# Optimization experiments

Hardware: AMD Instinct MI355X
Metric: run time of the kernel (lower is better)

Reference implementation:

```python
import jax, jax.numpy as jnp
import numpy as np

BN_EPS = 1e-5
Q_EPS = 1e-8

def quant_weight(w):
    # per-output-channel median-abs scale, ternary quantization
    s = jnp.median(jnp.abs(w).reshape(w.shape[0], -1), axis=1)
    s = jnp.maximum(s, Q_EPS)[:, None, None, None]
    return jnp.clip(jnp.round(w / s), -1.0, 1.0) * s

def bitconv(x, w, b, stride, pad):
    wq = quant_weight(w)
    y = jax.lax.conv_general_dilated(
        x, wq, (stride, stride), [(pad, pad), (pad, pad)],
        dimension_numbers=('NCHW', 'OIHW', 'NCHW'))
    return y + b[None, :, None, None]

def bn(x, g, b, m, v):
    scale = g / jnp.sqrt(v + BN_EPS)
    return x * scale[None, :, None, None] + (b - m * scale)[None, :, None, None]

def setup_inputs() -> dict:
    key = jax.random.key(0)
    ks = jax.random.split(key, 20)
    B, Cin, H, W = 64, 1024, 14, 14
    width, Cout = 256, 1024  # planes=256, expansion=4
    d = {}
    d['x'] = jax.random.normal(ks[0], (B, Cin, H, W), jnp.float32)
    d['w1'] = jax.random.normal(ks[1], (width, Cin, 1, 1), jnp.float32) * 0.05
    d['b1'] = jax.random.normal(ks[2], (width,), jnp.float32) * 0.01
    d['g1'] = jax.random.uniform(ks[3], (width,), jnp.float32, 0.5, 1.5)
    d['be1'] = jax.random.normal(ks[4], (width,), jnp.float32) * 0.1
    d['m1'] = jax.random.normal(ks[5], (width,), jnp.float32) * 0.1
    d['v1'] = jax.random.uniform(ks[6], (width,), jnp.float32, 0.5, 1.5)
    d['w2'] = jax.random.normal(ks[7], (width, width, 3, 3), jnp.float32) * 0.05
    d['b2'] = jax.random.normal(ks[8], (width,), jnp.float32) * 0.01
    d['g2'] = jax.random.uniform(ks[9], (width,), jnp.float32, 0.5, 1.5)
    d['be2'] = jax.random.normal(ks[10], (width,), jnp.float32) * 0.1
    d['m2'] = jax.random.normal(ks[11], (width,), jnp.float32) * 0.1
    d['v2'] = jax.random.uniform(ks[12], (width,), jnp.float32, 0.5, 1.5)
    d['w3'] = jax.random.normal(ks[13], (Cout, width, 1, 1), jnp.float32) * 0.05
    d['b3'] = jax.random.normal(ks[14], (Cout,), jnp.float32) * 0.01
    d['g3'] = jax.random.uniform(ks[15], (Cout,), jnp.float32, 0.5, 1.5)
    d['be3'] = jax.random.normal(ks[16], (Cout,), jnp.float32) * 0.1
    d['m3'] = jax.random.normal(ks[17], (Cout,), jnp.float32) * 0.1
    d['v3'] = jax.random.uniform(ks[18], (Cout,), jnp.float32, 0.5, 1.5)
    return d

def reference(x, w1, b1, g1, be1, m1, v1,
              w2, b2, g2, be2, m2, v2,
              w3, b3, g3, be3, m3, v3):
    out = jax.nn.silu(bn(bitconv(x, w1, b1, 1, 0), g1, be1, m1, v1))
    out = jax.nn.silu(bn(bitconv(out, w2, b2, 1, 1), g2, be2, m2, v2))
    out = bn(bitconv(out, w3, b3, 1, 0), g3, be3, m3, v3)
    return jax.nn.silu(out + x)
```

## Files before the change

### kernel.cpp

```cpp
#include <hip/hip_runtime.h>
#include <cstdint>
#include <cstddef>

typedef unsigned short u16;
typedef unsigned int u32;
typedef __attribute__((ext_vector_type(4))) float f32x4;
typedef __attribute__((ext_vector_type(8))) short s16x8;

__device__ __forceinline__ u16 f2bf(float f) {
  u32 u = __float_as_uint(f);
  u = (u + 0x7fffu + ((u >> 16) & 1u)) >> 16;
  return (u16)u;
}

__device__ __forceinline__ float silu_f(float y) {
  return y / (1.0f + __expf(-y));
}

__device__ __forceinline__ void gl_lds16(const u16* g, u16* l) {
  __builtin_amdgcn_global_load_lds(
      (const __attribute__((address_space(1))) void*)g,
      (__attribute__((address_space(3))) void*)l, 16, 0, 0);
}

template<int N, int REMAP>
__global__ __launch_bounds__(64) void quant_kernel(
    const float* __restrict__ w, const float* __restrict__ bias,
    const float* __restrict__ g, const float* __restrict__ be,
    const float* __restrict__ mu, const float* __restrict__ var,
    u16* __restrict__ wq, float* __restrict__ alpha, float* __restrict__ beta)
{
  constexpr int NV = N / 64;
  __shared__ int hist[256];

  const int lane = threadIdx.x;
  const int ch = blockIdx.x;

  u32 vals[NV];
  const float* wp = w + (size_t)ch * N;
  #pragma unroll
  for (int t = 0; t < NV; ++t)
    vals[t] = __float_as_uint(wp[lane + 64 * t]);

  const int r0 = N / 2;
  int r = r0;
  u32 prefix = 0;
  #pragma unroll
  for (int pass = 0; pass < 4; ++pass) {
    const int shift = 24 - 8 * pass;
    hist[lane] = 0;
    hist[64 + lane] = 0;
    hist[128 + lane] = 0;
    hist[192 + lane] = 0;
    __syncthreads();
    #pragma unroll
    for (int t = 0; t < NV; ++t) {
      u32 a = vals[t] & 0x7fffffffu;
      bool cand;
      if (pass == 0) cand = true;
      else cand = ((a >> (shift + 8)) == (prefix >> (shift + 8)));
      if (cand) atomicAdd(&hist[(a >> shift) & 255], 1);
    }
    __syncthreads();
    int h0 = hist[4 * lane + 0];
    int h1 = hist[4 * lane + 1];
    int h2 = hist[4 * lane + 2];
    int h3 = hist[4 * lane + 3];
    int s4 = h0 + h1 + h2 + h3;
    int cum = s4;
    #pragma unroll
    for (int off = 1; off < 64; off <<= 1) {
      int tt = __shfl_up(cum, off);
      if (lane >= off) cum += tt;
    }
    int pre = cum - s4;
    bool sel = (r > pre) && (r <= cum);
    unsigned long long bal = __ballot(sel);
    int src = __ffsll((unsigned long long)bal) - 1;
    int c0 = pre + h0, c1 = c0 + h1, c2 = c1 + h2;
    int d_l, nr_l;
    if (r <= c0)      { d_l = 4 * lane + 0; nr_l = r - pre; }
    else if (r <= c1) { d_l = 4 * lane + 1; nr_l = r - c0; }
    else if (r <= c2) { d_l = 4 * lane + 2; nr_l = r - c1; }
    else              { d_l = 4 * lane + 3; nr_l = r - c2; }
    int d = __shfl(d_l, src);
    r = __shfl(nr_l, src);
    prefix |= (u32)d << shift;
    __syncthreads();
  }
  const u32 v0 = prefix;

  int cle = 0;
  u32 mn = 0xFFFFFFFFu;
  #pragma unroll
  for (int t = 0; t < NV; ++t) {
    u32 a = vals[t] & 0x7fffffffu;
    cle += (a <= v0) ? 1 : 0;
    if (a > v0) mn = min(mn, a);
  }
  #pragma unroll
  for (int off = 1; off < 64; off <<= 1) {
    cle += __shfl_xor(cle, off);
    mn = min(mn, (u32)__shfl_xor((int)mn, off));
  }
  u32 v1 = (cle >= r0 + 1) ? v0 : mn;

  float s = 0.5f * (__uint_as_float(v0) + __uint_as_float(v1));
  s = fmaxf(s, 1e-8f);

  #pragma unroll
  for (int t = 0; t < NV; ++t) {
    int i = lane + 64 * t;
    float q = rintf(__uint_as_float(vals[t]) / s);
    q = fminf(fmaxf(q, -1.0f), 1.0f);
    int oi;
    if (REMAP) {
      int cin = i / 9, tap = i - cin * 9;
      oi = tap * 256 + cin;
    } else {
      oi = i;
    }
    wq[(size_t)ch * N + oi] = f2bf(q);
  }
  if (lane == 0) {
    float sc = g[ch] / sqrtf(var[ch] + 1e-5f);
    alpha[ch] = s * sc;
    beta[ch] = (bias[ch] - mu[ch]) * sc + be[ch];
  }
}

__global__ __launch_bounds__(256) void transpose_cast_kernel(
    const float* __restrict__ x, u16* __restrict__ xb)
{
  __shared__ u16 tile[64 * 198];
  const int n = blockIdx.x;
  const int c0 = blockIdx.y * 64;
  const float* xp = x + ((size_t)n * 1024 + c0) * 196;
  const float4* xp4 = reinterpret_cast<const float4*>(xp);
  for (int i = threadIdx.x; i < 64 * 49; i += 256) {
    int c = i / 49, hg = i - c * 49;
    float4 v = xp4[i];
    u16* t = &tile[c * 198 + hg * 4];
    t[0] = f2bf(v.x); t[1] = f2bf(v.y); t[2] = f2bf(v.z); t[3] = f2bf(v.w);
  }
  __syncthreads();
  u32* op = reinterpret_cast<u32*>(xb + (size_t)n * 196 * 1024 + c0);
  for (int i = threadIdx.x; i < 196 * 32; i += 256) {
    int hw = i >> 5, cp = i & 31;
    u32 lo = tile[(cp * 2) * 198 + hw];
    u32 hi = tile[(cp * 2 + 1) * 198 + hw];
    op[hw * 512 + cp] = lo | (hi << 16);
  }
}

template<int MODE, int KTOT, int BJ>
__global__ __launch_bounds__(256, 2) void gemm_kernel(
    const u16* __restrict__ Wq, const u16* __restrict__ Bact,
    const float* __restrict__ alpha, const float* __restrict__ beta,
    u16* __restrict__ outb, float* __restrict__ outf, const float* __restrict__ xres)
{
  constexpr int BK = 64;
  constexpr int NKT = KTOT / BK;
  constexpr int NI = BJ / 32;
  constexpr int ACH = 4;
  constexpr int BCH = BJ / 32;
  constexpr int SMEM_SIZE = (MODE == 3) ? 34816 : 25600;

  __shared__ __align__(16) char smem[SMEM_SIZE];
  u16* As = (u16*)smem;
  u16* Bs = (u16*)(smem + 16384);
  float* aS = (float*)(MODE == 3 ? (smem + 33792) : (smem + 16384 + BJ * 128));
  float* bS = aS + 128;
  float* lbuf = (float*)smem;

  const int tid = threadIdx.x;
  const int jb = blockIdx.x * BJ;
  const int cb = blockIdx.y * 128;
  const int wave = tid >> 6;
  const int lane = tid & 63;
  const int wm = (wave & 1) * 64;
  const int wn = (wave >> 1) * (BJ / 2);
  const int quad = lane >> 4;
  const int l16 = lane & 15;
  const int lr = lane >> 3;
  const int perm = (lane & 7) ^ lr;

  const u16* gA[ACH];
  #pragma unroll
  for (int it = 0; it < ACH; ++it) {
    int row = wave * 32 + it * 8 + lr;
    gA[it] = Wq + (size_t)(cb + row) * KTOT + perm * 8;
  }
  const u16* gB[BCH];
  #pragma unroll
  for (int it = 0; it < BCH; ++it) {
    int row = wave * (8 * BCH) + it * 8 + lr;
    if (MODE == 2) {
      int j = jb + row;
      int n = j / 196, hw = j - n * 196;
      int h = hw / 14, w = hw - h * 14;
      gB[it] = Bact + (size_t)(((n * 16 + h) * 16 + w) * 256) + perm * 8;
    } else {
      gB[it] = Bact + (size_t)(jb + row) * KTOT + perm * 8;
    }
  }

  if (tid < 128) {
    aS[tid] = alpha[cb + tid];
    bS[tid] = beta[cb + tid];
  }

  f32x4 acc[4][NI];
  #pragma unroll
  for (int a = 0; a < 4; ++a)
    #pragma unroll
    for (int b = 0; b < NI; ++b)
      acc[a][b] = {0.f, 0.f, 0.f, 0.f};

  for (int kt = 0; kt < NKT; ++kt) {
    #pragma unroll
    for (int it = 0; it < ACH; ++it)
      gl_lds16(gA[it] + kt * BK, As + (wave * ACH + it) * 512);
    if (MODE == 2) {
      int tap = kt >> 2;
      int c0 = (kt & 3) * 64;
      int dy = tap / 3, dx = tap - dy * 3;
      int tapoff = (dy * 16 + dx) * 256 + c0;
      #pragma unroll
      for (int it = 0; it < BCH; ++it)
        gl_lds16(gB[it] + tapoff, Bs + (wave * BCH + it) * 512);
    } else {
      #pragma unroll
      for (int it = 0; it < BCH; ++it)
        gl_lds16(gB[it] + kt * BK, Bs + (wave * BCH + it) * 512);
    }
    __syncthreads();

    #pragma unroll
    for (int s = 0; s < 2; ++s) {
      s16x8 af[4], bf[NI];
      #pragma unroll
      for (int mi = 0; mi < 4; ++mi) {
        int row = wm + mi * 16 + l16;
        int kc = s * 4 + quad;
        af[mi] = *reinterpret_cast<const s16x8*>(&As[row * BK + ((kc ^ (row & 7)) << 3)]);
      }
      #pragma unroll
      for (int ni = 0; ni < NI; ++ni) {
        int row = wn + ni * 16 + l16;
        int kc = s * 4 + quad;
        bf[ni] = *reinterpret_cast<const s16x8*>(&Bs[row * BK + ((kc ^ (row & 7)) << 3)]);
      }
      #pragma unroll
      for (int mi = 0; mi < 4; ++mi)
        #pragma unroll
        for (int ni = 0; ni < NI; ++ni)
          acc[mi][ni] = __builtin_amdgcn_mfma_f32_16x16x32_bf16(af[mi], bf[ni], acc[mi][ni], 0, 0, 0);
    }
    __syncthreads();
  }

  if (MODE == 1 || MODE == 2) {
    #pragma unroll
    for (int mi = 0; mi < 4; ++mi) {
      const int lc = wm + mi * 16 + quad * 4;
      #pragma unroll
      for (int ni = 0; ni < NI; ++ni) {
        const int j = jb + wn + ni * 16 + l16;
        ushort4 pk;
        float y;
        y = silu_f(aS[lc + 0] * acc[mi][ni][0] + bS[lc + 0]); pk.x = f2bf(y);
        y = silu_f(aS[lc + 1] * acc[mi][ni][1] + bS[lc + 1]); pk.y = f2bf(y);
        y = silu_f(aS[lc + 2] * acc[mi][ni][2] + bS[lc + 2]); pk.z = f2bf(y);
        y = silu_f(aS[lc + 3] * acc[mi][ni][3] + bS[lc + 3]); pk.w = f2bf(y);
        size_t base;
        if (MODE == 1) {
          int n = j / 196, hw = j - n * 196;
          int h = hw / 14, w = hw - h * 14;
          base = (size_t)(((n * 16 + h + 1) * 16) + (w + 1)) * 256 + cb + lc;
        } else {
          base = (size_t)j * 256 + cb + lc;
        }
        *reinterpret_cast<ushort4*>(&outb[base]) = pk;
      }
    }
  } else {
    #pragma unroll
    for (int k = 0; k < 2; ++k) {
      if ((wave & 1) == k) {
        #pragma unroll
        for (int mi = 0; mi < 4; ++mi) {
          const int cl = mi * 16 + quad * 4;
          const int gc = 64 * k + cl;
          #pragma unroll
          for (int ni = 0; ni < 4; ++ni) {
            const int jj = wn + ni * 16 + l16;
            #pragma unroll
            for (int r = 0; r < 4; ++r)
              lbuf[(cl + r) * 132 + jj] = aS[gc + r] * acc[mi][ni][r] + bS[gc + r];
          }
        }
      }
      __syncthreads();
      #pragma unroll
      for (int it = 0; it < 8; ++it) {
        int idx = tid + it * 256;
        int cl = idx >> 5;
        int jg = idx & 31;
        int c = cb + 64 * k + cl;
        int j0 = jb + jg * 4;
        int n = j0 / 196, hw = j0 - n * 196;
        size_t o = (size_t)n * 200704 + (size_t)c * 196 + hw;
        float4 lv = *reinterpret_cast<float4*>(&lbuf[cl * 132 + jg * 4]);
        float4 xv = *reinterpret_cast<const float4*>(&xres[o]);
        float4 ov;
        ov.x = silu_f(lv.x + xv.x);
        ov.y = silu_f(lv.y + xv.y);
        ov.z = silu_f(lv.z + xv.z);
        ov.w = silu_f(lv.w + xv.w);
        *reinterpret_cast<float4*>(&outf[o]) = ov;
      }
      __syncthreads();
    }
  }
}

extern "C" void kernel_launch(void* const* d_in, const int* in_sizes, int n_in,
                              void* d_out, int out_size, void* d_ws, size_t ws_size,
                              hipStream_t stream)
{
  const float* x   = (const float*)d_in[0];
  const float* w1  = (const float*)d_in[1];
  const float* b1  = (const float*)d_in[2];
  const float* g1  = (const float*)d_in[3];
  const float* be1 = (const float*)d_in[4];
  const float* m1  = (const float*)d_in[5];
  const float* v1  = (const float*)d_in[6];
  const float* w2  = (const float*)d_in[7];
  const float* b2  = (const float*)d_in[8];
  const float* g2  = (const float*)d_in[9];
  const float* be2 = (const float*)d_in[10];
  const float* m2  = (const float*)d_in[11];
  const float* v2  = (const float*)d_in[12];
  const float* w3  = (const float*)d_in[13];
  const float* b3  = (const float*)d_in[14];
  const float* g3  = (const float*)d_in[15];
  const float* be3 = (const float*)d_in[16];
  const float* m3  = (const float*)d_in[17];
  const float* v3  = (const float*)d_in[18];
  float* out = (float*)d_out;

  uint8_t* ws = (uint8_t*)d_ws;
  u16* xb    = (u16*)(ws);
  u16* act1p = (u16*)(ws + 25690112ull);
  u16* act2  = (u16*)(ws + 34078720ull);
  u16* w1q   = (u16*)(ws + 40501248ull);
  u16* w2q   = (u16*)(ws + 41025536ull);
  u16* w3q   = (u16*)(ws + 42205184ull);
  float* a1c = (float*)(ws + 42729472ull);
  float* b1c = a1c + 256;
  float* a2c = b1c + 256;
  float* b2c = a2c + 256;
  float* a3c = b2c + 256;
  float* b3c = a3c + 1024;

  hipMemsetAsync(act1p, 0, 8388608ull, stream);

  transpose_cast_kernel<<<dim3(64, 16), 256, 0, stream>>>(x, xb);
  quant_kernel<1024, 0><<<256, 64, 0, stream>>>(w1, b1, g1, be1, m1, v1, w1q, a1c, b1c);
  quant_kernel<2304, 1><<<256, 64, 0, stream>>>(w2, b2, g2, be2, m2, v2, w2q, a2c, b2c);
  quant_kernel<256, 0><<<1024, 64, 0, stream>>>(w3, b3, g3, be3, m3, v3, w3q, a3c, b3c);

  gemm_kernel<1, 1024, 64><<<dim3(196, 2), 256, 0, stream>>>(w1q, xb, a1c, b1c, act1p, (float*)nullptr, (const float*)nullptr);
  gemm_kernel<2, 2304, 64><<<dim3(196, 2), 256, 0, stream>>>(w2q, act1p, a2c, b2c, act2, (float*)nullptr, (const float*)nullptr);
  gemm_kernel<3, 256, 128><<<dim3(98, 8), 256, 0, stream>>>(w3q, act2, a3c, b3c, (u16*)nullptr, out, x);
}
```

Baseline: 239.5 us.

## Fuse prep kernels into one launch, zero only halo, shrink GEMM tiles

```diff
diff --git a/kernel.cpp b/kernel.cpp
--- a/kernel.cpp
+++ b/kernel.cpp
@@ -24,17 +24,16 @@
 }
 
 template<int N, int REMAP>
-__global__ __launch_bounds__(64) void quant_kernel(
+__device__ void quant_dev(
+    int grp, int wave, int lane, int* hist ,
     const float* __restrict__ w, const float* __restrict__ bias,
     const float* __restrict__ g, const float* __restrict__ be,
     const float* __restrict__ mu, const float* __restrict__ var,
     u16* __restrict__ wq, float* __restrict__ alpha, float* __restrict__ beta)
 {
   constexpr int NV = N / 64;
-  __shared__ int hist[256];
-
-  const int lane = threadIdx.x;
-  const int ch = blockIdx.x;
+  const int ch = grp * 4 + wave;
+  const int wb = wave * 256;
 
   u32 vals[NV];
   const float* wp = w + (size_t)ch * N;
@@ -48,10 +47,10 @@
   #pragma unroll
   for (int pass = 0; pass < 4; ++pass) {
     const int shift = 24 - 8 * pass;
-    hist[lane] = 0;
-    hist[64 + lane] = 0;
-    hist[128 + lane] = 0;
-    hist[192 + lane] = 0;
+    hist[wb + lane] = 0;
+    hist[wb + 64 + lane] = 0;
+    hist[wb + 128 + lane] = 0;
+    hist[wb + 192 + lane] = 0;
     __syncthreads();
     #pragma unroll
     for (int t = 0; t < NV; ++t) {
@@ -59,13 +58,13 @@
       bool cand;
       if (pass == 0) cand = true;
       else cand = ((a >> (shift + 8)) == (prefix >> (shift + 8)));
-      if (cand) atomicAdd(&hist[(a >> shift) & 255], 1);
-    }
-    __syncthreads();
-    int h0 = hist[4 * lane + 0];
-    int h1 = hist[4 * lane + 1];
-    int h2 = hist[4 * lane + 2];
-    int h3 = hist[4 * lane + 3];
+      if (cand) atomicAdd(&hist[wb + ((a >> shift) & 255)], 1);
+    }
+    __syncthreads();
+    int h0 = hist[wb + 4 * lane + 0];
+    int h1 = hist[wb + 4 * lane + 1];
+    int h2 = hist[wb + 4 * lane + 2];
+    int h3 = hist[wb + 4 * lane + 3];
     int s4 = h0 + h1 + h2 + h3;
     int cum = s4;
     #pragma unroll
@@ -129,32 +128,74 @@
   }
 }
 
-__global__ __launch_bounds__(256) void transpose_cast_kernel(
-    const float* __restrict__ x, u16* __restrict__ xb)
+__global__ __launch_bounds__(256) void prep_kernel(
+    const float* __restrict__ x, u16* __restrict__ xb,
+    const float* __restrict__ w1, const float* __restrict__ b1,
+    const float* __restrict__ g1, const float* __restrict__ be1,
+    const float* __restrict__ m1, const float* __restrict__ v1,
+    u16* __restrict__ w1q, float* __restrict__ a1c, float* __restrict__ b1c,
+    const float* __restrict__ w2, const float* __restrict__ b2,
+    const float* __restrict__ g2, const float* __restrict__ be2,
+    const float* __restrict__ m2, const float* __restrict__ v2,
+    u16* __restrict__ w2q, float* __restrict__ a2c, float* __restrict__ b2c,
+    const float* __restrict__ w3, const float* __restrict__ b3,
+    const float* __restrict__ g3, const float* __restrict__ be3,
+    const float* __restrict__ m3, const float* __restrict__ v3,
+    u16* __restrict__ w3q, float* __restrict__ a3c, float* __restrict__ b3c,
+    u16* __restrict__ act1p)
 {
-  __shared__ u16 tile[64 * 198];
-  const int n = blockIdx.x;
-  const int c0 = blockIdx.y * 64;
-  const float* xp = x + ((size_t)n * 1024 + c0) * 196;
-  const float4* xp4 = reinterpret_cast<const float4*>(xp);
-  for (int i = threadIdx.x; i < 64 * 49; i += 256) {
-    int c = i / 49, hg = i - c * 49;
-    float4 v = xp4[i];
-    u16* t = &tile[c * 198 + hg * 4];
-    t[0] = f2bf(v.x); t[1] = f2bf(v.y); t[2] = f2bf(v.z); t[3] = f2bf(v.w);
-  }
-  __syncthreads();
-  u32* op = reinterpret_cast<u32*>(xb + (size_t)n * 196 * 1024 + c0);
-  for (int i = threadIdx.x; i < 196 * 32; i += 256) {
-    int hw = i >> 5, cp = i & 31;
-    u32 lo = tile[(cp * 2) * 198 + hw];
-    u32 hi = tile[(cp * 2 + 1) * 198 + hw];
-    op[hw * 512 + cp] = lo | (hi << 16);
+  __shared__ __align__(16) char smem[25344];
+  const int b = blockIdx.x;
+  const int tid = threadIdx.x;
+  const int wave = tid >> 6;
+  const int lane = tid & 63;
+
+  if (b < 1024) {
+    u16* tile = (u16*)smem;
+    const int n = b >> 4;
+    const int c0 = (b & 15) * 64;
+    const float* xp = x + ((size_t)n * 1024 + c0) * 196;
+    const float4* xp4 = reinterpret_cast<const float4*>(xp);
+    for (int i = tid; i < 64 * 49; i += 256) {
+      int c = i / 49, hg = i - c * 49;
+      float4 v = xp4[i];
+      u16* t = &tile[c * 198 + hg * 4];
+      t[0] = f2bf(v.x); t[1] = f2bf(v.y); t[2] = f2bf(v.z); t[3] = f2bf(v.w);
+    }
+    __syncthreads();
+    u32* op = reinterpret_cast<u32*>(xb + (size_t)n * 196 * 1024 + c0);
+    for (int i = tid; i < 196 * 32; i += 256) {
+      int hw = i >> 5, cp = i & 31;
+      u32 lo = tile[(cp * 2) * 198 + hw];
+      u32 hi = tile[(cp * 2 + 1) * 198 + hw];
+      op[hw * 512 + cp] = lo | (hi << 16);
+    }
+  } else if (b < 1088) {
+    quant_dev<1024, 0>(b - 1024, wave, lane, (int*)smem,
+                       w1, b1, g1, be1, m1, v1, w1q, a1c, b1c);
+  } else if (b < 1152) {
+    quant_dev<2304, 1>(b - 1088, wave, lane, (int*)smem,
+                       w2, b2, g2, be2, m2, v2, w2q, a2c, b2c);
+  } else if (b < 1408) {
+    quant_dev<256, 0>(b - 1152, wave, lane, (int*)smem,
+                      w3, b3, g3, be3, m3, v3, w3q, a3c, b3c);
+  } else {
+    const int n = b - 1408;
+    u32* base = reinterpret_cast<u32*>(act1p + (size_t)n * 16 * 16 * 256);
+    for (int i = tid; i < 7680; i += 256) {
+      int p = i >> 7;
+      int cc = i & 127;
+      int h, w;
+      if (p < 16)      { h = 0;  w = p; }
+      else if (p < 32) { h = 15; w = p - 16; }
+      else { int q = p - 32; h = 1 + (q >> 1); w = (q & 1) * 15; }
+      base[((h * 16 + w) << 7) + cc] = 0u;
+    }
   }
 }
 
 template<int MODE, int KTOT, int BJ>
-__global__ __launch_bounds__(256, 2) void gemm_kernel(
+__global__ __launch_bounds__(256, 4) void gemm_kernel(
     const u16* __restrict__ Wq, const u16* __restrict__ Bact,
     const float* __restrict__ alpha, const float* __restrict__ beta,
     u16* __restrict__ outb, float* __restrict__ outf, const float* __restrict__ xres)
@@ -164,7 +205,7 @@
   constexpr int NI = BJ / 32;
   constexpr int ACH = 4;
   constexpr int BCH = BJ / 32;
-  constexpr int SMEM_SIZE = (MODE == 3) ? 34816 : 25600;
+  constexpr int SMEM_SIZE = (MODE == 3) ? 34816 : (16384 + BJ * 128 + 1024);
 
   __shared__ __align__(16) char smem[SMEM_SIZE];
   u16* As = (u16*)smem;
@@ -364,14 +405,14 @@
   float* a3c = b2c + 256;
   float* b3c = a3c + 1024;
 
-  hipMemsetAsync(act1p, 0, 8388608ull, stream);
-
-  transpose_cast_kernel<<<dim3(64, 16), 256, 0, stream>>>(x, xb);
-  quant_kernel<1024, 0><<<256, 64, 0, stream>>>(w1, b1, g1, be1, m1, v1, w1q, a1c, b1c);
-  quant_kernel<2304, 1><<<256, 64, 0, stream>>>(w2, b2, g2, be2, m2, v2, w2q, a2c, b2c);
-  quant_kernel<256, 0><<<1024, 64, 0, stream>>>(w3, b3, g3, be3, m3, v3, w3q, a3c, b3c);
-
-  gemm_kernel<1, 1024, 64><<<dim3(196, 2), 256, 0, stream>>>(w1q, xb, a1c, b1c, act1p, (float*)nullptr, (const float*)nullptr);
-  gemm_kernel<2, 2304, 64><<<dim3(196, 2), 256, 0, stream>>>(w2q, act1p, a2c, b2c, act2, (float*)nullptr, (const float*)nullptr);
+  prep_kernel<<<1472, 256, 0, stream>>>(
+      x, xb,
+      w1, b1, g1, be1, m1, v1, w1q, a1c, b1c,
+      w2, b2, g2, be2, m2, v2, w2q, a2c, b2c,
+      w3, b3, g3, be3, m3, v3, w3q, a3c, b3c,
+      act1p);
+
+  gemm_kernel<1, 1024, 32><<<dim3(392, 2), 256, 0, stream>>>(w1q, xb, a1c, b1c, act1p, (float*)nullptr, (const float*)nullptr);
+  gemm_kernel<2, 2304, 32><<<dim3(392, 2), 256, 0, stream>>>(w2q, act1p, a2c, b2c, act2, (float*)nullptr, (const float*)nullptr);
   gemm_kernel<3, 256, 128><<<dim3(98, 8), 256, 0, stream>>>(w3q, act2, a3c, b3c, (u16*)nullptr, out, x);
 }
```

Measured after the change: 227.4 us. 5.1% less time.
